# Optimization experiments

Measured on AMD Instinct MI355X. Metric: run time of the kernel, lower is better.

## Reference

```python
import jax, jax.numpy as jnp
import numpy as np

NUM_WIRES = 512
BATCH = 65536
HBAR = 2.0  # PennyLane default.gaussian convention; sqrt(2*hbar) = 2


def setup_inputs() -> dict:
    key = jax.random.key(0)
    ks = jax.random.split(key, 8)
    state_batch = jax.random.normal(ks[0], (BATCH, NUM_WIRES), dtype=jnp.float32)
    squeeze = jax.random.normal(ks[1], (NUM_WIRES,), dtype=jnp.float32)
    phase = jax.random.normal(ks[2], (NUM_WIRES,), dtype=jnp.float32)
    disp = jax.random.normal(ks[3], (NUM_WIRES,), dtype=jnp.float32)
    squeeze2 = jax.random.normal(ks[4], (NUM_WIRES,), dtype=jnp.float32)
    kerr = jax.random.normal(ks[5], (NUM_WIRES,), dtype=jnp.float32)
    head_w = jax.random.normal(ks[6], (1, NUM_WIRES), dtype=jnp.float32) / np.sqrt(NUM_WIRES)
    head_b = jnp.zeros((1,), dtype=jnp.float32)
    return {
        "state_batch": state_batch,
        "squeeze": squeeze,
        "phase": phase,
        "disp": disp,
        "squeeze2": squeeze2,
        "kerr": kerr,
        "head_w": head_w,
        "head_b": head_b,
    }


def _cv_features(x, squeeze, phase, disp, squeeze2):
    # Gaussian-state mean propagation per wire, vacuum start, hbar=2.
    # S(r,0): xbar *= e^-r ; R(phi): xbar' = xbar*cos(phi) (pbar=0 before rotation)
    # D(d,0): xbar += 2d ; S(r2,0): xbar *= e^-r2
    # Kerr is non-Gaussian: identity on the Gaussian mean vector (unsupported on
    # default.gaussian; omitted from the quadrature-mean evolution).
    # expval(X) = xbar
    root2h = np.sqrt(2.0 * HBAR)  # = 2
    return jnp.exp(-squeeze2) * (root2h * x * jnp.exp(-squeeze) * jnp.cos(phase) + root2h * disp)


def reference(state_batch, squeeze, phase, disp, squeeze2, kerr, head_w, head_b):
    x = state_batch[:, :NUM_WIRES]  # torch.real of a real tensor is identity
    feats = _cv_features(x, squeeze, phase, disp, squeeze2)  # [B, W]
    out = feats @ head_w.T + head_b  # [B, 1]
    return out.squeeze(-1)
```

## Files before the change

### kernel.cpp

```cpp
#include <hip/hip_runtime.h>
#include <hip/hip_bf16.h>
#include <math.h>

#define NUM_WIRES 512

__global__ __launch_bounds__(256, 8) void fused_dot_kernel(
        const float* __restrict__ x,
        const float* __restrict__ squeeze,
        const float* __restrict__ phase,
        const float* __restrict__ disp,
        const float* __restrict__ squeeze2,
        const float* __restrict__ head_w,
        const float* __restrict__ head_b,
        float* __restrict__ out, int rows) {
    __shared__ float s_coeff[NUM_WIRES];
    __shared__ float s_red[256];

    const int t = threadIdx.x;
    float partial = 0.0f;
    #pragma unroll
    for (int k = 0; k < 2; ++k) {
        const int j = t + k * 256;
        const float e2 = expf(-squeeze2[j]);
        const float w  = head_w[j];
        s_coeff[j] = w * 2.0f * e2 * expf(-squeeze[j]) * cosf(phase[j]);
        partial += w * 2.0f * e2 * disp[j];
    }
    s_red[t] = partial;
    __syncthreads();
    #pragma unroll
    for (int s = 128; s > 0; s >>= 1) {
        if (t < s) s_red[t] += s_red[t + s];
        __syncthreads();
    }
    const float bias = s_red[0] + head_b[0];

    const int lane = t & 63;
    const int wave = t >> 6;
    const float4 c0 = *reinterpret_cast<const float4*>(&s_coeff[lane * 4]);
    const float4 c1 = *reinterpret_cast<const float4*>(&s_coeff[256 + lane * 4]);

    const int waveId = blockIdx.x * 4 + wave;
    const int base = waveId * 8;
    #pragma unroll
    for (int i = 0; i < 4; ++i) {
        const int r0 = base + 2 * i;
        if (r0 + 1 >= rows + 1) break;
        const float4* p0 = reinterpret_cast<const float4*>(x + (size_t)r0 * NUM_WIRES);
        const float4* p1 = reinterpret_cast<const float4*>(x + (size_t)(r0 + 1) * NUM_WIRES);
        const float4 a0 = p0[lane];
        const float4 b0 = p0[64 + lane];
        const float4 a1 = p1[lane];
        const float4 b1 = p1[64 + lane];
        float s0 = a0.x * c0.x + a0.y * c0.y + a0.z * c0.z + a0.w * c0.w
                 + b0.x * c1.x + b0.y * c1.y + b0.z * c1.z + b0.w * c1.w;
        float s1 = a1.x * c0.x + a1.y * c0.y + a1.z * c0.z + a1.w * c0.w
                 + b1.x * c1.x + b1.y * c1.y + b1.z * c1.z + b1.w * c1.w;
        #pragma unroll
        for (int off = 32; off >= 1; off >>= 1) {
            s0 += __shfl_xor(s0, off, 64);
            s1 += __shfl_xor(s1, off, 64);
        }
        if (lane == 0) out[r0] = s0 + bias;
        if (lane == 1 && r0 + 1 < rows) out[r0 + 1] = s1 + bias;
    }
}

extern "C" void kernel_launch(void* const* d_in, const int* in_sizes, int n_in,
                              void* d_out, int out_size, void* d_ws, size_t ws_size,
                              hipStream_t stream) {
    const float* state_batch = (const float*)d_in[0];
    const float* squeeze     = (const float*)d_in[1];
    const float* phase       = (const float*)d_in[2];
    const float* disp        = (const float*)d_in[3];
    const float* squeeze2    = (const float*)d_in[4];
    const float* head_w      = (const float*)d_in[6];
    const float* head_b      = (const float*)d_in[7];
    float* out = (float*)d_out;

    fused_dot_kernel<<<2048, 256, 0, stream>>>(state_batch, squeeze, phase, disp,
                                               squeeze2, head_w, head_b, out, out_size);
}
```

Baseline: 26.76 us.

## Compute coefficients per wave, use nontemporal loads and transpose-style shuffle reduction

Each wave now computes the per-wire coefficients and bias term directly in registers from vector loads, which removes the LDS staging and the block-wide syncthreads reduction. The row data is fetched with nontemporal loads, eight float4 loads in flight per batch of four rows. The per-row cross-lane reductions are merged into a butterfly that swaps partial sums between lanes, cutting the number of shuffles. Occupancy hint is lowered to 4 blocks per CU, and every wave redoes the transcendental coefficient math.

```diff
diff --git a/kernel.cpp b/kernel.cpp
--- a/kernel.cpp
+++ b/kernel.cpp
@@ -4,7 +4,18 @@
 
 #define NUM_WIRES 512
 
-__global__ __launch_bounds__(256, 8) void fused_dot_kernel(
+typedef float f4 __attribute__((ext_vector_type(4)));
+
+__device__ __forceinline__ f4 ntload(const f4* p) {
+    return __builtin_nontemporal_load(p);
+}
+
+__device__ __forceinline__ float dot8(f4 a, f4 b, f4 ca, f4 cb) {
+    return a[0]*ca[0] + a[1]*ca[1] + a[2]*ca[2] + a[3]*ca[3]
+         + b[0]*cb[0] + b[1]*cb[1] + b[2]*cb[2] + b[3]*cb[3];
+}
+
+__global__ __launch_bounds__(256, 4) void fused_dot_kernel(
         const float* __restrict__ x,
         const float* __restrict__ squeeze,
         const float* __restrict__ phase,
@@ -13,56 +24,68 @@
         const float* __restrict__ head_w,
         const float* __restrict__ head_b,
         float* __restrict__ out, int rows) {
-    __shared__ float s_coeff[NUM_WIRES];
-    __shared__ float s_red[256];
-
     const int t = threadIdx.x;
-    float partial = 0.0f;
-    #pragma unroll
-    for (int k = 0; k < 2; ++k) {
-        const int j = t + k * 256;
-        const float e2 = expf(-squeeze2[j]);
-        const float w  = head_w[j];
-        s_coeff[j] = w * 2.0f * e2 * expf(-squeeze[j]) * cosf(phase[j]);
-        partial += w * 2.0f * e2 * disp[j];
-    }
-    s_red[t] = partial;
-    __syncthreads();
-    #pragma unroll
-    for (int s = 128; s > 0; s >>= 1) {
-        if (t < s) s_red[t] += s_red[t + s];
-        __syncthreads();
-    }
-    const float bias = s_red[0] + head_b[0];
-
     const int lane = t & 63;
     const int wave = t >> 6;
-    const float4 c0 = *reinterpret_cast<const float4*>(&s_coeff[lane * 4]);
-    const float4 c1 = *reinterpret_cast<const float4*>(&s_coeff[256 + lane * 4]);
-
     const int waveId = blockIdx.x * 4 + wave;
     const int base = waveId * 8;
+    if (base >= rows) return;
+
+    const f4 sqa = ((const f4*)squeeze )[lane], sqb = ((const f4*)squeeze )[64 + lane];
+    const f4 pha = ((const f4*)phase   )[lane], phb = ((const f4*)phase   )[64 + lane];
+    const f4 dia = ((const f4*)disp    )[lane], dib = ((const f4*)disp    )[64 + lane];
+    const f4 s2a = ((const f4*)squeeze2)[lane], s2b = ((const f4*)squeeze2)[64 + lane];
+    const f4 wa  = ((const f4*)head_w  )[lane], wb  = ((const f4*)head_w  )[64 + lane];
+
+    f4 c0, c1;
+    float part = 0.0f;
     #pragma unroll
-    for (int i = 0; i < 4; ++i) {
-        const int r0 = base + 2 * i;
-        if (r0 + 1 >= rows + 1) break;
-        const float4* p0 = reinterpret_cast<const float4*>(x + (size_t)r0 * NUM_WIRES);
-        const float4* p1 = reinterpret_cast<const float4*>(x + (size_t)(r0 + 1) * NUM_WIRES);
-        const float4 a0 = p0[lane];
-        const float4 b0 = p0[64 + lane];
-        const float4 a1 = p1[lane];
-        const float4 b1 = p1[64 + lane];
-        float s0 = a0.x * c0.x + a0.y * c0.y + a0.z * c0.z + a0.w * c0.w
-                 + b0.x * c1.x + b0.y * c1.y + b0.z * c1.z + b0.w * c1.w;
-        float s1 = a1.x * c0.x + a1.y * c0.y + a1.z * c0.z + a1.w * c0.w
-                 + b1.x * c1.x + b1.y * c1.y + b1.z * c1.z + b1.w * c1.w;
-        #pragma unroll
-        for (int off = 32; off >= 1; off >>= 1) {
-            s0 += __shfl_xor(s0, off, 64);
-            s1 += __shfl_xor(s1, off, 64);
+    for (int k = 0; k < 4; ++k) {
+        const float e2a = expf(-s2a[k]);
+        const float e2b = expf(-s2b[k]);
+        c0[k] = wa[k] * 2.0f * e2a * expf(-sqa[k]) * cosf(pha[k]);
+        c1[k] = wb[k] * 2.0f * e2b * expf(-sqb[k]) * cosf(phb[k]);
+        part += wa[k] * 2.0f * e2a * dia[k] + wb[k] * 2.0f * e2b * dib[k];
+    }
+    #pragma unroll
+    for (int off = 32; off >= 1; off >>= 1)
+        part += __shfl_xor(part, off, 64);
+    const float bias = part + head_b[0];
+
+    const f4* xb = (const f4*)(x + (size_t)base * NUM_WIRES);
+    #pragma unroll
+    for (int i = 0; i < 2; ++i) {
+        const int r0 = base + i * 4;
+        const f4* p = xb + (size_t)i * 4 * 128;
+        const f4 a0 = ntload(p +        lane), b0 = ntload(p +  64 + lane);
+        const f4 a1 = ntload(p + 128 +  lane), b1 = ntload(p + 192 + lane);
+        const f4 a2 = ntload(p + 256 +  lane), b2 = ntload(p + 320 + lane);
+        const f4 a3 = ntload(p + 384 +  lane), b3 = ntload(p + 448 + lane);
+
+        float s0 = dot8(a0, b0, c0, c1);
+        float s1 = dot8(a1, b1, c0, c1);
+        float s2 = dot8(a2, b2, c0, c1);
+        float s3 = dot8(a3, b3, c0, c1);
+
+        s0 += __shfl_xor(s0, 32, 64);
+        s1 += __shfl_xor(s1, 32, 64);
+        s2 += __shfl_xor(s2, 32, 64);
+        s3 += __shfl_xor(s3, 32, 64);
+        float u0 = (lane & 32) ? s1 : s0;
+        float u1 = (lane & 32) ? s3 : s2;
+        u0 += __shfl_xor(u0, 16, 64);
+        u1 += __shfl_xor(u1, 16, 64);
+        float v = (lane & 16) ? u1 : u0;
+        v += __shfl_xor(v, 8, 64);
+        v += __shfl_xor(v, 4, 64);
+        v += __shfl_xor(v, 2, 64);
+        v += __shfl_xor(v, 1, 64);
+
+        if ((lane & 15) == 0) {
+            const int roff = ((lane >> 4) & 1) * 2 + (lane >> 5);
+            const int r = r0 + roff;
+            if (r < rows) out[r] = v + bias;
         }
-        if (lane == 0) out[r0] = s0 + bias;
-        if (lane == 1 && r0 + 1 < rows) out[r0 + 1] = s1 + bias;
     }
 }
 
```

Result: no change. 26.29 us (median of 2 runs) (-1.8%).
